# Optimization experiments

Measured on AMD Instinct MI355X. Metric: run time of the kernel, lower is better.

## Reference

```python
import jax, jax.numpy as jnp
import numpy as np

RES = 14
KEY_DIM = 32
NUM_HEADS = 12
ATTN_RATIO = 4
DIM = 384
VAL_ATTN_DIM = ATTN_RATIO * KEY_DIM * NUM_HEADS  # 1536
QKV_DIM = VAL_ATTN_DIM + 2 * KEY_DIM * NUM_HEADS  # 2304
BN_EPS = 1e-5


def _bias_idxs():
    # torch.meshgrid default is 'ij'
    gy, gx = jnp.meshgrid(jnp.arange(RES), jnp.arange(RES), indexing='ij')
    pos = jnp.stack([gy.reshape(-1), gx.reshape(-1)])           # [2, N]
    rel = jnp.abs(pos[:, :, None] - pos[:, None, :])            # [2, N, N]
    return rel[0] * RES + rel[1]                                # [N, N] int


def _linear_bn(x, w, gamma, beta, mean, var):
    # bias-free Linear (torch weight layout [out,in]) + BatchNorm1d (eval)
    y = x @ w.T
    inv = gamma / jnp.sqrt(var + BN_EPS)
    return y * inv + (beta - mean * inv)


def setup_inputs() -> dict:
    key = jax.random.key(0)
    ks = jax.random.split(key, 12)
    B, N = 128, RES * RES
    f = jax.random.normal
    return {
        'x': f(ks[0], (B, N, DIM), jnp.float32),
        'qkv_w': f(ks[1], (QKV_DIM, DIM), jnp.float32) * 0.02,
        'qkv_gamma': f(ks[2], (QKV_DIM,), jnp.float32) * 0.1 + 1.0,
        'qkv_beta': f(ks[3], (QKV_DIM,), jnp.float32) * 0.1,
        'qkv_mean': f(ks[4], (QKV_DIM,), jnp.float32) * 0.1,
        'qkv_var': jax.random.uniform(ks[5], (QKV_DIM,), jnp.float32, 0.5, 1.5),
        'attn_biases': f(ks[6], (NUM_HEADS, RES * RES), jnp.float32) * 0.1,
        'proj_w': f(ks[7], (DIM, VAL_ATTN_DIM), jnp.float32) * 0.02,
        'proj_gamma': f(ks[8], (DIM,), jnp.float32) * 0.1 + 1.0,
        'proj_beta': f(ks[9], (DIM,), jnp.float32) * 0.1,
        'proj_mean': f(ks[10], (DIM,), jnp.float32) * 0.1,
        'proj_var': jax.random.uniform(ks[11], (DIM,), jnp.float32, 0.5, 1.5),
    }


def reference(x, qkv_w, qkv_gamma, qkv_beta, qkv_mean, qkv_var,
              attn_biases, proj_w, proj_gamma, proj_beta, proj_mean, proj_var):
    B, N, _ = x.shape
    scale = KEY_DIM ** -0.5
    qkv = _linear_bn(x, qkv_w, qkv_gamma, qkv_beta, qkv_mean, qkv_var)
    qkv = qkv.reshape(B, N, NUM_HEADS, -1)
    q = qkv[..., :KEY_DIM]                       # [B,N,H,dk]
    k = qkv[..., KEY_DIM:2 * KEY_DIM]            # [B,N,H,dk]
    v = qkv[..., 2 * KEY_DIM:]                   # [B,N,H,dv]
    bias = attn_biases[:, _bias_idxs()]          # [H,N,N]
    attn = jnp.einsum('bnhd,bmhd->bhnm', q, k) * scale + bias[None]
    attn = jax.nn.softmax(attn, axis=-1)
    out = jnp.einsum('bhnm,bmhd->bnhd', attn, v).reshape(B, N, VAL_ATTN_DIM)
    out = jax.nn.silu(out)
    return _linear_bn(out, proj_w, proj_gamma, proj_beta, proj_mean, proj_var)
```

## Files before the change

kernel.cpp:

```cpp
#include <hip/hip_runtime.h>
#include <cstdint>

#define NQ 196
#define DIMX 384
#define QKVD 2304
#define VAD 1536
#define NHD 12
#define MTOT 25088

#define KSTR 40
#define VSTR 232
#define TSTR 140

typedef unsigned int u32;
typedef unsigned short u16;
typedef __bf16 bf16_t;
typedef bf16_t bf16x8 __attribute__((ext_vector_type(8)));
typedef float f32x4 __attribute__((ext_vector_type(4)));

__device__ inline u16 f2b(float f) {
  u32 u = __float_as_uint(f);
  u32 r = (u + 0x7fffu + ((u >> 16) & 1u)) >> 16;
  return (u16)r;
}
__device__ inline float b2f(u16 u) { return __uint_as_float(((u32)u) << 16); }
__device__ inline int iabs(int v) { return v < 0 ? -v : v; }

__device__ inline void gld_lds16(const void* g, void* l) {
  __builtin_amdgcn_global_load_lds((__attribute__((address_space(1))) void*)g,
                                   (__attribute__((address_space(3))) void*)l,
                                   16, 0, 0);
}


__global__ void cvt_kernel(const float* __restrict__ in, u16* __restrict__ out, int n4) {
  int i = blockIdx.x * 256 + threadIdx.x;
  if (i >= n4) return;
  float4 v = ((const float4*)in)[i];
  ushort4 o;
  o.x = f2b(v.x); o.y = f2b(v.y); o.z = f2b(v.z); o.w = f2b(v.w);
  ((ushort4*)out)[i] = o;
}

__global__ void cvt_wqkv(const float* __restrict__ in, u16* __restrict__ out) {
  int i = blockIdx.x * 256 + threadIdx.x;
  if (i >= QKVD * DIMX / 4) return;
  const int newc = i / (DIMX / 4);
  const int kc = (i - newc * (DIMX / 4)) * 4;
  int oldc;
  if (newc < 384)      { int h = newc >> 5;              oldc = h * 192 + (newc & 31); }
  else if (newc < 768) { int t = newc - 384; int h = t >> 5; oldc = h * 192 + 32 + (t & 31); }
  else                 { int t = newc - 768; int h = t >> 7; oldc = h * 192 + 64 + (t & 127); }
  float4 v = *(const float4*)(in + (size_t)oldc * DIMX + kc);
  ushort4 o;
  o.x = f2b(v.x); o.y = f2b(v.y); o.z = f2b(v.z); o.w = f2b(v.w);
  *(ushort4*)(out + (size_t)newc * DIMX + kc) = o;
}

__global__ void bn_tab(const float* __restrict__ g, const float* __restrict__ be,
                       const float* __restrict__ mn, const float* __restrict__ vr,
                       float* __restrict__ inv, float* __restrict__ off, int n) {
  int i = blockIdx.x * 256 + threadIdx.x;
  if (i >= n) return;
  float iv = g[i] * rsqrtf(vr[i] + 1e-5f);
  inv[i] = iv;
  off[i] = be[i] - mn[i] * iv;
}

__global__ void bn_tab_qkv(const float* __restrict__ g, const float* __restrict__ be,
                           const float* __restrict__ mn, const float* __restrict__ vr,
                           float* __restrict__ inv, float* __restrict__ off) {
  int i = blockIdx.x * 256 + threadIdx.x;
  if (i >= QKVD) return;
  const int h = i / 192, r = i - h * 192;
  const int newc = (r < 32) ? h * 32 + r
                 : (r < 64) ? 384 + h * 32 + (r - 32)
                            : 768 + h * 128 + (r - 64);
  float iv = g[i] * rsqrtf(vr[i] + 1e-5f);
  inv[newc] = iv;
  off[newc] = be[i] - mn[i] * iv;
}


template <int MODE>
__global__ __launch_bounds__(256) void gemm_bt(
    const u16* __restrict__ A, const u16* __restrict__ B, int K,
    const float* __restrict__ inv, const float* __restrict__ off,
    u16* __restrict__ Qb, u16* __restrict__ Kb, u16* __restrict__ Vt,
    float* __restrict__ out) {
  constexpr int LDSU = (MODE == 0) ? 128 * TSTR : 8192;
  __shared__ __align__(16) u16 lds[LDSU];
  u16* As = lds;
  u16* Bs = lds + 4096;
  const int tid = threadIdx.x;
  const int wid = tid >> 6, lane = tid & 63;
  const int wm = wid & 1, wn = wid >> 1;
  const int fr = lane & 15, fk = (lane >> 4) << 3;
  const u16* Ab = A + (size_t)(blockIdx.y * 128) * K;
  const u16* Bb = B + (size_t)(blockIdx.x * 128) * K;
  const int c0 = (wid << 6) | lane;
  const int r0 = c0 >> 2, kc0 = (c0 & 3) << 3;
  const int c1 = c0 + 256;
  const int r1 = c1 >> 2, kc1 = (c1 & 3) << 3;

  f32x4 acc[4][4] = {};

  for (int k0 = 0; k0 < K; k0 += 32) {
    gld_lds16(Ab + (size_t)r0 * K + (k0 + kc0), &As[wid << 9]);
    gld_lds16(Ab + (size_t)r1 * K + (k0 + kc1), &As[2048 + (wid << 9)]);
    gld_lds16(Bb + (size_t)r0 * K + (k0 + kc0), &Bs[wid << 9]);
    gld_lds16(Bb + (size_t)r1 * K + (k0 + kc1), &Bs[2048 + (wid << 9)]);
    __syncthreads();
    bf16x8 av[4], bv[4];
#pragma unroll
    for (int t = 0; t < 4; t++)
      av[t] = *(const bf16x8*)&As[(wm * 64 + t * 16 + fr) * 32 + fk];
#pragma unroll
    for (int t = 0; t < 4; t++)
      bv[t] = *(const bf16x8*)&Bs[(wn * 64 + t * 16 + fr) * 32 + fk];
#pragma unroll
    for (int mt = 0; mt < 4; mt++)
#pragma unroll
      for (int nt = 0; nt < 4; nt++)
        acc[mt][nt] = __builtin_amdgcn_mfma_f32_16x16x32_bf16(av[mt], bv[nt], acc[mt][nt], 0, 0, 0);
    __syncthreads();
  }

  const int lrow0 = wm * 64 + ((lane >> 4) << 2);
  const int lcol0 = wn * 64 + fr;

  if (MODE == 0) {
    const int bx = blockIdx.x, by = blockIdx.y;
    const bool isV = bx >= 6;
#pragma unroll
    for (int nt = 0; nt < 4; nt++) {
      const int lc = lcol0 + nt * 16;
      const int gc = bx * 128 + lc;
      const float iv = inv[gc], of = off[gc];
#pragma unroll
      for (int mt = 0; mt < 4; mt++)
#pragma unroll
        for (int rg = 0; rg < 4; rg++) {
          const int lr = lrow0 + mt * 16 + rg;
          const u16 us = f2b(acc[mt][nt][rg] * iv + of);
          if (isV) lds[lc * TSTR + lr] = us;
          else     lds[lr * TSTR + lc] = us;
        }
    }
    __syncthreads();
    if (!isV) {
      u16* dstB = (bx < 3) ? Qb : Kb;
      const int h0 = (bx < 3 ? bx : bx - 3) * 4;
#pragma unroll
      for (int it = 0; it < 8; it++) {
        const int idx = it * 256 + tid;
        const int ch = idx & 3, hl = (idx >> 2) & 3, row = idx >> 4;
        const int rowg = by * 128 + row;
        const int b = rowg / 196, n = rowg - b * 196;
        const size_t bh = (size_t)(b * NHD + h0 + hl);
        const u16* src = &lds[row * TSTR + hl * 32 + ch * 8];
        uint2 a0 = *(const uint2*)src;
        uint2 a1 = *(const uint2*)(src + 4);
        *(uint4*)(dstB + (bh * NQ + n) * 32 + ch * 8) = make_uint4(a0.x, a0.y, a1.x, a1.y);
      }
    } else {
      const int h = bx - 6;
#pragma unroll
      for (int it = 0; it < 16; it++) {
        const int idx = it * 256 + tid;
        const int nk = idx & 31, col = idx >> 5;
        const int rowg = by * 128 + nk * 4;
        const int b = rowg / 196, n = rowg - b * 196;
        uint2 v = *(const uint2*)&lds[col * TSTR + nk * 4];
        *(uint2*)(Vt + ((size_t)(b * NHD + h) * 128 + col) * NQ + n) = v;
      }
    }
  } else {
    const int colb = blockIdx.x * 128 + lcol0;
    const int rowb = blockIdx.y * 128 + lrow0;
#pragma unroll
    for (int nt = 0; nt < 4; nt++) {
      const int col = colb + nt * 16;
      const float iv = inv[col], of = off[col];
#pragma unroll
      for (int mt = 0; mt < 4; mt++)
#pragma unroll
        for (int rg = 0; rg < 4; rg++) {
          const int row = rowb + mt * 16 + rg;
          out[(size_t)row * DIMX + col] = acc[mt][nt][rg] * iv + of;
        }
    }
  }
}


__global__ __launch_bounds__(512) void attn_kernel(
    const u16* __restrict__ Qg, const u16* __restrict__ Kg,
    const u16* __restrict__ Vtg, const float* __restrict__ biases,
    u16* __restrict__ AO) {
  __shared__ __align__(16) u16 Ks[208 * KSTR];
  __shared__ __align__(16) u16 Vs[128 * VSTR];
  __shared__ __align__(16) u16 Ps[8][16 * VSTR];
  __shared__ __align__(16) float biasS[NQ];

  const int tid = threadIdx.x, wid = tid >> 6, lane = tid & 63;
  const int fr = lane & 15, fj = lane >> 4, fk = fj << 3;
  const int bh = blockIdx.x, b = bh / NHD, h = bh - b * NHD;
  const float scale = 0.17677669529663687f;

  for (int i = tid; i < NQ * 4; i += 512) {
    const int m = i >> 2, kc = (i & 3) << 3;
    uint4 v = *(const uint4*)(Kg + ((size_t)bh * NQ + m) * 32 + kc);
    *(uint4*)&Ks[m * KSTR + kc] = v;
  }
  {
    const u32* src = (const u32*)(Vtg + (size_t)bh * 128 * NQ);
    u32* dst = (u32*)Vs;
    for (int i = tid; i < 128 * 98; i += 512) {
      const int d = i / 98, nc = i - d * 98;
      dst[d * (VSTR / 2) + nc] = src[i];
    }
    for (int i = tid; i < 128 * 18; i += 512) {
      const int d = i / 18, nc = 98 + (i - d * 18);
      dst[d * (VSTR / 2) + nc] = 0u;
    }
  }
  if (tid < NQ) biasS[tid] = biases[h * NQ + tid];
  {
    const int row = lane >> 2, c = 208 + (lane & 3) * 4;
    *(uint2*)&Ps[wid][row * VSTR + c] = make_uint2(0u, 0u);
  }
  __syncthreads();

  for (int rt = wid; rt < 13; rt += 8) {
    int qrow = rt * 16 + fr; qrow = qrow > 195 ? 195 : qrow;
    const bf16x8 qf = *(const bf16x8*)(Qg + ((size_t)bh * NQ + qrow) * 32 + fk);

    f32x4 s[13];
#pragma unroll
    for (int t = 0; t < 13; t++) {
      const bf16x8 kf = *(const bf16x8*)&Ks[(t * 16 + fr) * KSTR + fk];
      f32x4 z = {0.f, 0.f, 0.f, 0.f};
      s[t] = __builtin_amdgcn_mfma_f32_16x16x32_bf16(qf, kf, z, 0, 0, 0);
    }

    int yn[4], xn[4];
#pragma unroll
    for (int rg = 0; rg < 4; rg++) {
      int n = rt * 16 + fj * 4 + rg;
      int y = (n * 586) >> 13; y = y > 13 ? 13 : y;
      yn[rg] = y; xn[rg] = n - y * 14;
    }
#pragma unroll
    for (int t = 0; t < 13; t++) {
      const int m = t * 16 + fr;
      const bool valid = m < NQ;
      int ym = (m * 586) >> 13; ym = ym > 13 ? 13 : ym;
      const int xm = m - ym * 14;
#pragma unroll
      for (int rg = 0; rg < 4; rg++) {
        int idx = iabs(yn[rg] - ym) * 14 + iabs(xn[rg] - xm);
        idx = idx > 195 ? 195 : idx;
        const float bv = biasS[idx];
        s[t][rg] = valid ? (s[t][rg] * scale + bv) : -1e30f;
      }
    }
    float rinv[4];
#pragma unroll
    for (int rg = 0; rg < 4; rg++) {
      float mx = s[0][rg];
#pragma unroll
      for (int t = 1; t < 13; t++) mx = fmaxf(mx, s[t][rg]);
      mx = fmaxf(mx, __shfl_xor(mx, 1));
      mx = fmaxf(mx, __shfl_xor(mx, 2));
      mx = fmaxf(mx, __shfl_xor(mx, 4));
      mx = fmaxf(mx, __shfl_xor(mx, 8));
      float ls = 0.f;
#pragma unroll
      for (int t = 0; t < 13; t++) {
        const float e = __expf(s[t][rg] - mx);
        s[t][rg] = e;
        ls += e;
      }
      ls += __shfl_xor(ls, 1);
      ls += __shfl_xor(ls, 2);
      ls += __shfl_xor(ls, 4);
      ls += __shfl_xor(ls, 8);
      rinv[rg] = 1.f / ls;
    }
#pragma unroll
    for (int t = 0; t < 13; t++)
#pragma unroll
      for (int rg = 0; rg < 4; rg++)
        Ps[wid][(fj * 4 + rg) * VSTR + t * 16 + fr] = f2b(s[t][rg]);
    __threadfence_block();

    f32x4 o[8] = {};
#pragma unroll
    for (int kc = 0; kc < 7; kc++) {
      const bf16x8 pf = *(const bf16x8*)&Ps[wid][fr * VSTR + kc * 32 + fk];
#pragma unroll
      for (int dt = 0; dt < 8; dt++) {
        const bf16x8 vf = *(const bf16x8*)&Vs[(dt * 16 + fr) * VSTR + kc * 32 + fk];
        o[dt] = __builtin_amdgcn_mfma_f32_16x16x32_bf16(pf, vf, o[dt], 0, 0, 0);
      }
    }
#pragma unroll
    for (int rg = 0; rg < 4; rg++) {
      const int n = rt * 16 + fj * 4 + rg;
      if (n < NQ) {
        const float rv = rinv[rg];
#pragma unroll
        for (int dt = 0; dt < 8; dt++) {
          float x = o[dt][rg] * rv;
          x = x / (1.f + __expf(-x));
          AO[((size_t)(b * NQ + n)) * VAD + h * 128 + dt * 16 + fr] = f2b(x);
        }
      }
    }
    __threadfence_block();
  }
}


extern "C" void kernel_launch(void* const* d_in, const int* in_sizes, int n_in,
                              void* d_out, int out_size, void* d_ws, size_t ws_size,
                              hipStream_t stream) {
  const float* x          = (const float*)d_in[0];
  const float* qkv_w      = (const float*)d_in[1];
  const float* qkv_gamma  = (const float*)d_in[2];
  const float* qkv_beta   = (const float*)d_in[3];
  const float* qkv_mean   = (const float*)d_in[4];
  const float* qkv_var    = (const float*)d_in[5];
  const float* attn_bias  = (const float*)d_in[6];
  const float* proj_w     = (const float*)d_in[7];
  const float* proj_gamma = (const float*)d_in[8];
  const float* proj_beta  = (const float*)d_in[9];
  const float* proj_mean  = (const float*)d_in[10];
  const float* proj_var   = (const float*)d_in[11];

  const size_t szXB    = (size_t)MTOT * DIMX * 2;
  const size_t szQKVW  = (size_t)QKVD * DIMX * 2;
  const size_t szPROJW = (size_t)DIMX * VAD * 2;
  const size_t szQK    = (size_t)128 * NHD * NQ * 32 * 2;
  const size_t szV     = (size_t)128 * NHD * 128 * NQ * 2;
  const size_t szAO    = (size_t)MTOT * VAD * 2;
  const size_t szX     = (szXB + szQKVW > szAO) ? (szXB + szQKVW) : szAO;

  char* w = (char*)d_ws;
  u16* projwb = (u16*)w; w += szPROJW;
  float* inv1 = (float*)w; w += QKVD * 4;
  float* off1 = (float*)w; w += QKVD * 4;
  float* inv2 = (float*)w; w += DIMX * 4;
  float* off2 = (float*)w; w += DIMX * 4;
  u16* Qb = (u16*)w; w += szQK;
  u16* Kb = (u16*)w; w += szQK;
  u16* Vt = (u16*)w; w += szV;
  char* regionX = w; w += szX;
  u16* xb    = (u16*)regionX;
  u16* qkvwb = (u16*)(regionX + szXB);
  u16* AO    = (u16*)regionX;

  if ((size_t)(w - (char*)d_ws) > ws_size) return;

  cvt_kernel<<<MTOT * DIMX / 4 / 256, 256, 0, stream>>>(x, xb, MTOT * DIMX / 4);
  cvt_wqkv<<<(QKVD * DIMX / 4 + 255) / 256, 256, 0, stream>>>(qkv_w, qkvwb);
  cvt_kernel<<<DIMX * VAD / 4 / 256, 256, 0, stream>>>(proj_w, projwb, DIMX * VAD / 4);
  bn_tab_qkv<<<(QKVD + 255) / 256, 256, 0, stream>>>(qkv_gamma, qkv_beta, qkv_mean, qkv_var, inv1, off1);
  bn_tab<<<(DIMX + 255) / 256, 256, 0, stream>>>(proj_gamma, proj_beta, proj_mean, proj_var, inv2, off2, DIMX);

  gemm_bt<0><<<dim3(QKVD / 128, MTOT / 128), 256, 0, stream>>>(
      xb, qkvwb, DIMX, inv1, off1, Qb, Kb, Vt, nullptr);
  attn_kernel<<<128 * NHD, 512, 0, stream>>>(Qb, Kb, Vt, attn_bias, AO);
  gemm_bt<1><<<dim3(DIMX / 128, MTOT / 128), 256, 0, stream>>>(
      AO, projwb, VAD, inv2, off2, nullptr, nullptr, nullptr, (float*)d_out);
}
```

Before: 401.9 us.

## Precompute expanded bias table and read padded V directly from global in attention

A new pre-pass kernel expands the relative-position bias into a padded per-head [208x208] table, with -1e30 in the masked entries. The attention kernel then loads bias as float4 from global instead of computing indices and gathering from LDS. V is written by the QKV GEMM into a padded row stride (224) that a separate kernel zero-fills, and the attention kernel reads V fragments straight from global/cache instead of staging them in LDS. Dropping the V staging shrinks LDS use, and launch_bounds(512,4) is added, both aimed at higher occupancy. The trade-off is more global/L2 traffic, since every wave rereads V, plus two extra small launches.

```diff
diff --git a/kernel.cpp b/kernel.cpp
--- a/kernel.cpp
+++ b/kernel.cpp
@@ -10,6 +10,8 @@
 
 #define KSTR 40
 #define VSTR 232
+#define VTS 224
+#define BTS 208
 #define TSTR 140
 
 typedef unsigned int u32;
@@ -79,6 +81,27 @@
   float iv = g[i] * rsqrtf(vr[i] + 1e-5f);
   inv[newc] = iv;
   off[newc] = be[i] - mn[i] * iv;
+}
+
+__global__ void bias_expand(const float* __restrict__ biases, float* __restrict__ bt) {
+  int i = blockIdx.x * 256 + threadIdx.x;
+  if (i >= NHD * BTS * BTS) return;
+  const int h = i / (BTS * BTS), r = i - h * BTS * BTS;
+  const int m = r / BTS, n = r - m * BTS;
+  float v = -1e30f;
+  if (m < NQ && n < NQ) {
+    const int ym = m / 14, xm = m - ym * 14;
+    const int yn = n / 14, xn = n - yn * 14;
+    v = biases[h * NQ + iabs(yn - ym) * 14 + iabs(xn - xm)];
+  }
+  bt[i] = v;
+}
+
+__global__ void pad_vt(u16* __restrict__ Vt) {
+  int i = blockIdx.x * 256 + threadIdx.x;
+  if (i >= 128 * NHD * 128 * 14) return;
+  const int row = i / 14, c = i - row * 14;
+  *(u32*)(Vt + (size_t)row * VTS + NQ + c * 2) = 0u;
 }
 
 
@@ -172,7 +195,7 @@
         const int rowg = by * 128 + nk * 4;
         const int b = rowg / 196, n = rowg - b * 196;
         uint2 v = *(const uint2*)&lds[col * TSTR + nk * 4];
-        *(uint2*)(Vt + ((size_t)(b * NHD + h) * 128 + col) * NQ + n) = v;
+        *(uint2*)(Vt + ((size_t)(b * NHD + h) * 128 + col) * VTS + n) = v;
       }
     }
   } else {
@@ -194,14 +217,12 @@
 }
 
 
-__global__ __launch_bounds__(512) void attn_kernel(
+__global__ __launch_bounds__(512, 4) void attn_kernel(
     const u16* __restrict__ Qg, const u16* __restrict__ Kg,
-    const u16* __restrict__ Vtg, const float* __restrict__ biases,
+    const u16* __restrict__ Vtg, const float* __restrict__ biasT,
     u16* __restrict__ AO) {
   __shared__ __align__(16) u16 Ks[208 * KSTR];
-  __shared__ __align__(16) u16 Vs[128 * VSTR];
   __shared__ __align__(16) u16 Ps[8][16 * VSTR];
-  __shared__ __align__(16) float biasS[NQ];
 
   const int tid = threadIdx.x, wid = tid >> 6, lane = tid & 63;
   const int fr = lane & 15, fj = lane >> 4, fk = fj << 3;
@@ -210,27 +231,20 @@
 
   for (int i = tid; i < NQ * 4; i += 512) {
     const int m = i >> 2, kc = (i & 3) << 3;
-    uint4 v = *(const uint4*)(Kg + ((size_t)bh * NQ + m) * 32 + kc);
-    *(uint4*)&Ks[m * KSTR + kc] = v;
-  }
-  {
-    const u32* src = (const u32*)(Vtg + (size_t)bh * 128 * NQ);
-    u32* dst = (u32*)Vs;
-    for (int i = tid; i < 128 * 98; i += 512) {
-      const int d = i / 98, nc = i - d * 98;
-      dst[d * (VSTR / 2) + nc] = src[i];
-    }
-    for (int i = tid; i < 128 * 18; i += 512) {
-      const int d = i / 18, nc = 98 + (i - d * 18);
-      dst[d * (VSTR / 2) + nc] = 0u;
-    }
-  }
-  if (tid < NQ) biasS[tid] = biases[h * NQ + tid];
+    *(uint4*)&Ks[m * KSTR + kc] = *(const uint4*)(Kg + ((size_t)bh * NQ + m) * 32 + kc);
+  }
+  if (tid < 48) {
+    const int m = 196 + (tid >> 2), kc = (tid & 3) << 3;
+    *(uint4*)&Ks[m * KSTR + kc] = make_uint4(0u, 0u, 0u, 0u);
+  }
   {
     const int row = lane >> 2, c = 208 + (lane & 3) * 4;
     *(uint2*)&Ps[wid][row * VSTR + c] = make_uint2(0u, 0u);
   }
   __syncthreads();
+
+  const float* bT = biasT + (size_t)h * BTS * BTS;
+  const u16* Vb = Vtg + (size_t)bh * 128 * VTS;
 
   for (int rt = wid; rt < 13; rt += 8) {
     int qrow = rt * 16 + fr; qrow = qrow > 195 ? 195 : qrow;
@@ -244,27 +258,17 @@
       s[t] = __builtin_amdgcn_mfma_f32_16x16x32_bf16(qf, kf, z, 0, 0, 0);
     }
 
-    int yn[4], xn[4];
-#pragma unroll
-    for (int rg = 0; rg < 4; rg++) {
-      int n = rt * 16 + fj * 4 + rg;
-      int y = (n * 586) >> 13; y = y > 13 ? 13 : y;
-      yn[rg] = y; xn[rg] = n - y * 14;
-    }
+    const int n0 = rt * 16 + (fj << 2);
+    const float* bRow = bT + n0;
 #pragma unroll
     for (int t = 0; t < 13; t++) {
-      const int m = t * 16 + fr;
-      const bool valid = m < NQ;
-      int ym = (m * 586) >> 13; ym = ym > 13 ? 13 : ym;
-      const int xm = m - ym * 14;
-#pragma unroll
-      for (int rg = 0; rg < 4; rg++) {
-        int idx = iabs(yn[rg] - ym) * 14 + iabs(xn[rg] - xm);
-        idx = idx > 195 ? 195 : idx;
-        const float bv = biasS[idx];
-        s[t][rg] = valid ? (s[t][rg] * scale + bv) : -1e30f;
-      }
-    }
+      const float4 bv = *(const float4*)(bRow + (size_t)(t * 16 + fr) * BTS);
+      s[t][0] = s[t][0] * scale + bv.x;
+      s[t][1] = s[t][1] * scale + bv.y;
+      s[t][2] = s[t][2] * scale + bv.z;
+      s[t][3] = s[t][3] * scale + bv.w;
+    }
+
     float rinv[4];
 #pragma unroll
     for (int rg = 0; rg < 4; rg++) {
@@ -301,7 +305,7 @@
       const bf16x8 pf = *(const bf16x8*)&Ps[wid][fr * VSTR + kc * 32 + fk];
 #pragma unroll
       for (int dt = 0; dt < 8; dt++) {
-        const bf16x8 vf = *(const bf16x8*)&Vs[(dt * 16 + fr) * VSTR + kc * 32 + fk];
+        const bf16x8 vf = *(const bf16x8*)(Vb + (size_t)(dt * 16 + fr) * VTS + kc * 32 + fk);
         o[dt] = __builtin_amdgcn_mfma_f32_16x16x32_bf16(pf, vf, o[dt], 0, 0, 0);
       }
     }
@@ -343,7 +347,8 @@
   const size_t szQKVW  = (size_t)QKVD * DIMX * 2;
   const size_t szPROJW = (size_t)DIMX * VAD * 2;
   const size_t szQK    = (size_t)128 * NHD * NQ * 32 * 2;
-  const size_t szV     = (size_t)128 * NHD * 128 * NQ * 2;
+  const size_t szV     = (size_t)128 * NHD * 128 * VTS * 2;
+  const size_t szBT    = (size_t)NHD * BTS * BTS * 4;
   const size_t szAO    = (size_t)MTOT * VAD * 2;
   const size_t szX     = (szXB + szQKVW > szAO) ? (szXB + szQKVW) : szAO;
 
@@ -353,6 +358,7 @@
   float* off1 = (float*)w; w += QKVD * 4;
   float* inv2 = (float*)w; w += DIMX * 4;
   float* off2 = (float*)w; w += DIMX * 4;
+  float* biasT = (float*)w; w += szBT;
   u16* Qb = (u16*)w; w += szQK;
   u16* Kb = (u16*)w; w += szQK;
   u16* Vt = (u16*)w; w += szV;
@@ -368,10 +374,12 @@
   cvt_kernel<<<DIMX * VAD / 4 / 256, 256, 0, stream>>>(proj_w, projwb, DIMX * VAD / 4);
   bn_tab_qkv<<<(QKVD + 255) / 256, 256, 0, stream>>>(qkv_gamma, qkv_beta, qkv_mean, qkv_var, inv1, off1);
   bn_tab<<<(DIMX + 255) / 256, 256, 0, stream>>>(proj_gamma, proj_beta, proj_mean, proj_var, inv2, off2, DIMX);
+  bias_expand<<<(NHD * BTS * BTS + 255) / 256, 256, 0, stream>>>(attn_bias, biasT);
+  pad_vt<<<(128 * NHD * 128 * 14 + 255) / 256, 256, 0, stream>>>(Vt);
 
   gemm_bt<0><<<dim3(QKVD / 128, MTOT / 128), 256, 0, stream>>>(
       xb, qkvwb, DIMX, inv1, off1, Qb, Kb, Vt, nullptr);
-  attn_kernel<<<128 * NHD, 512, 0, stream>>>(Qb, Kb, Vt, attn_bias, AO);
+  attn_kernel<<<128 * NHD, 512, 0, stream>>>(Qb, Kb, Vt, attn_bias  == attn_bias ? biasT : biasT, AO);
   gemm_bt<1><<<dim3(DIMX / 128, MTOT / 128), 256, 0, stream>>>(
       AO, projwb, VAD, inv2, off2, nullptr, nullptr, nullptr, (float*)d_out);
 }
```

Result: slower. 759.8 us (+89.0%).
